# Kernel tuning notes

Hardware: AMD Instinct MI355X
Metric: run time of the kernel (lower is better)

The kernel has to match this reference:

```python
import jax, jax.numpy as jnp
import numpy as np

N_NODES = 100000
D = 128
N_EDGES = 640000


def _spmm(edge_index, w, x, n):
    # out[i] = sum over edges (i<-j): w * x[j]
    src, dst = edge_index[0], edge_index[1]
    return jax.ops.segment_sum(w[:, None] * x[dst], src, num_segments=n)


def setup_inputs() -> dict:
    key = jax.random.key(0)
    ks = jax.random.split(key, 8)
    inp = {
        "index_vectors": jax.random.normal(ks[0], (N_NODES, D), dtype=jnp.float32),
        "edge_index1": jax.random.randint(ks[1], (2, N_EDGES), 0, N_NODES, dtype=jnp.int64),
        "w1": jnp.ones((N_EDGES,), dtype=jnp.float32),
        "edge_index2": jax.random.randint(ks[2], (2, N_EDGES), 0, N_NODES, dtype=jnp.int64),
        "w2": jnp.ones((N_EDGES,), dtype=jnp.float32),
        "edge_index3": jax.random.randint(ks[3], (2, N_EDGES), 0, N_NODES, dtype=jnp.int64),
        "w3": jnp.ones((N_EDGES,), dtype=jnp.float32),
        "zeroth": jax.random.uniform(ks[4], (1, 1), dtype=jnp.float32),
        "fst": jax.random.uniform(ks[5], (1, 1), dtype=jnp.float32),
        "snd": jax.random.uniform(ks[6], (1, 1), dtype=jnp.float32),
        "trd": jax.random.uniform(ks[7], (1, 1), dtype=jnp.float32),
    }
    return inp


def reference(index_vectors, edge_index1, w1, edge_index2, w2, edge_index3, w3,
              zeroth, fst, snd, trd):
    n = index_vectors.shape[0]
    # hop-1 context: A @ x
    fst_ctx = _spmm(edge_index1, w1, index_vectors, n)
    # hop-2 context: A^2 @ roll(x, 1, axis=1)   (permute_vecs=True)
    snd_ctx = _spmm(edge_index2, w2, jnp.roll(index_vectors, 1, axis=1), n)
    # hop-3 context: A^3 @ roll(x, 2, axis=1)
    trd_ctx = _spmm(edge_index3, w3, jnp.roll(index_vectors, 2, axis=1), n)

    # relu-normalized scalar order weights (get_orders)
    r0, r1, r2, r3 = (jax.nn.relu(zeroth), jax.nn.relu(fst),
                      jax.nn.relu(snd), jax.nn.relu(trd))
    tot = r0 + r1 + r2 + r3 + 1e-6
    r0, r1, r2, r3 = r0 / tot, r1 / tot, r2 / tot, r3 / tot

    # use_sign=False -> plain weighted combination
    return r0 * index_vectors + r1 * fst_ctx + r2 * snd_ctx + r3 * trd_ctx
```

## Files before the change

### kernel.cpp

```cpp
#include <hip/hip_runtime.h>

#define N_NODES 100000
#define D 128
#define N_EDGES 640000
#define TOT_EDGES (3 * N_EDGES)

#define NB   256
#define NPB  391
#define BCAP 9216
#define OVF_CAP 65536
#define EPB  3072
#define BINA_BLOCKS (TOT_EDGES / EPB)
#define EPT  (EPB / 256)

#define WS_OVFCNT 0
#define WS_BCUR   64
#define WS_BBASE  16448
#define WS_BNUM   17472
#define WS_OVF    18496
#define WS_TMP    1067072
#define WS_FREC   19941440
#define WS_OFFS   35301440
#define WS_TOTAL_F 35701444

__device__ __forceinline__ void load_r(const float* z0, const float* z1,
                                       const float* z2, const float* z3,
                                       float& r0, float& r1, float& r2, float& r3) {
    r0 = fmaxf(z0[0], 0.0f);
    r1 = fmaxf(z1[0], 0.0f);
    r2 = fmaxf(z2[0], 0.0f);
    r3 = fmaxf(z3[0], 0.0f);
    float inv = 1.0f / (r0 + r1 + r2 + r3 + 1e-6f);
    r0 *= inv; r1 *= inv; r2 *= inv; r3 *= inv;
}

__global__ void binA_kernel(const int* __restrict__ ei1, const float* __restrict__ w1,
                            const int* __restrict__ ei2, const float* __restrict__ w2,
                            const int* __restrict__ ei3, const float* __restrict__ w3,
                            const float* __restrict__ z0, const float* __restrict__ z1,
                            const float* __restrict__ z2, const float* __restrict__ z3,
                            int* __restrict__ bcur, int* __restrict__ ovf_count,
                            int4* __restrict__ ovf, int2* __restrict__ tmp) {
    __shared__ int hist[NB];
    __shared__ int base[NB];
    int t = threadIdx.x;
    hist[t] = 0;
    __syncthreads();

    int e0 = blockIdx.x * EPB;
    int rank[EPT];
    int bkt[EPT];

    for (int k = 0; k < EPT; ++k) {
        int e = e0 + t + k * 256;
        int set = e / N_EDGES;
        int idx = e - set * N_EDGES;
        const int* ei = (set == 0) ? ei1 : (set == 1) ? ei2 : ei3;
        int src = ei[idx];
        int b = src / NPB;
        bkt[k]  = b;
        rank[k] = atomicAdd(&hist[b], 1);
    }
    __syncthreads();

    {
        int h = hist[t];
        base[t] = h ? atomicAdd(&bcur[t * 16], h) : 0;
    }
    __syncthreads();

    float r0, r1, r2, r3;
    load_r(z0, z1, z2, z3, r0, r1, r2, r3);

    for (int k = 0; k < EPT; ++k) {
        int e = e0 + t + k * 256;
        int set = e / N_EDGES;
        int idx = e - set * N_EDGES;
        const int* ei;  const float* w;
        if      (set == 0) { ei = ei1; w = w1; }
        else if (set == 1) { ei = ei2; w = w2; }
        else               { ei = ei3; w = w3; }
        int src = ei[idx];
        int dst = ei[N_EDGES + idx];
        float rk = (set == 0) ? r1 : (set == 1) ? r2 : r3;
        float scale = rk * w[idx];
        int b = bkt[k];
        int local = src - b * NPB;
        int pos = base[b] + rank[k];
        int rx = dst | (set << 17) | (local << 19);
        if (pos < BCAP) {
            tmp[(size_t)b * BCAP + pos] = make_int2(rx, __float_as_int(scale));
        } else {
            int o = atomicAdd(ovf_count, 1);
            if (o < OVF_CAP) ovf[o] = make_int4(src, dst | (set << 17),
                                                __float_as_int(scale), 0);
        }
    }
}

__global__ void scanB_kernel(const int* __restrict__ bcur,
                             int* __restrict__ bbase, int* __restrict__ bnum,
                             int* __restrict__ offsets) {
    __shared__ int s[NB];
    int t = threadIdx.x;
    int n = bcur[t * 16];
    if (n > BCAP) n = BCAP;
    bnum[t] = n;
    s[t] = n;
    __syncthreads();
    for (int off = 1; off < NB; off <<= 1) {
        int v = (t >= off) ? s[t - off] : 0;
        __syncthreads();
        s[t] += v;
        __syncthreads();
    }
    bbase[t] = s[t] - n;
    if (t == NB - 1) offsets[N_NODES] = s[t];
}

__global__ void binB_kernel(const int2* __restrict__ tmp,
                            const int* __restrict__ bbase, const int* __restrict__ bnum,
                            int2* __restrict__ frecs, int* __restrict__ offsets) {
    __shared__ int d[512];
    __shared__ int s[512];
    __shared__ int cur[NPB];
    int b = blockIdx.x;
    int t = threadIdx.x;
    int n = bnum[b];
    int gbase = bbase[b];

    d[t] = 0; d[t + 256] = 0;
    __syncthreads();
    for (int i = t; i < n; i += 256) {
        int rx = tmp[(size_t)b * BCAP + i].x;
        atomicAdd(&d[(rx >> 19) & 0x1FF], 1);
    }
    __syncthreads();
    s[t] = d[t]; s[t + 256] = d[t + 256];
    __syncthreads();
    for (int off = 1; off < 512; off <<= 1) {
        int v0 = (t       >= off) ? s[t       - off] : 0;
        int v1 = (t + 256 >= off) ? s[t + 256 - off] : 0;
        __syncthreads();
        s[t] += v0; s[t + 256] += v1;
        __syncthreads();
    }
    int node0 = b * NPB;
    for (int l = t; l < NPB; l += 256) {
        int excl = s[l] - d[l];
        cur[l] = excl;
        int node = node0 + l;
        if (node < N_NODES) offsets[node] = gbase + excl;
    }
    __syncthreads();
    for (int i = t; i < n; i += 256) {
        int2 rec = tmp[(size_t)b * BCAP + i];
        int pos = atomicAdd(&cur[(rec.x >> 19) & 0x1FF], 1);
        frecs[gbase + pos] = make_int2(rec.x & 0x7FFFF, rec.y);
    }
}

__global__ void gatherd_kernel(const float* __restrict__ x,
                               const int* __restrict__ offsets,
                               const int2* __restrict__ recs,
                               const float* __restrict__ z0, const float* __restrict__ z1,
                               const float* __restrict__ z2, const float* __restrict__ z3,
                               float* __restrict__ out) {
    int wid  = (blockIdx.x * blockDim.x + threadIdx.x) >> 6;
    int lane = threadIdx.x & 63;
    if (wid >= N_NODES) return;

    float r0, r1, r2, r3;
    load_r(z0, z1, z2, z3, r0, r1, r2, r3);

    float2 xv = ((const float2*)(x + (size_t)wid * D))[lane];

    int beg = offsets[wid];
    int end = offsets[wid + 1];
    int count = end - beg;
    int cnt64 = (count < 64) ? count : 64;

    int2 myrec = make_int2(0, 0);
    if (lane < cnt64) myrec = recs[beg + lane];

    float2 a0 = {0.f, 0.f}, a1 = {0.f, 0.f}, a2 = {0.f, 0.f};

    int j = 0;
    for (; j + 3 < cnt64; j += 4) {
        int rxa = __shfl(myrec.x, j),     rya = __shfl(myrec.y, j);
        int rxb = __shfl(myrec.x, j + 1), ryb = __shfl(myrec.y, j + 1);
        int rxc = __shfl(myrec.x, j + 2), ryc = __shfl(myrec.y, j + 2);
        int rxd = __shfl(myrec.x, j + 3), ryd = __shfl(myrec.y, j + 3);
        float2 va = ((const float2*)(x + (size_t)(rxa & 0x1FFFF) * D))[lane];
        float2 vb = ((const float2*)(x + (size_t)(rxb & 0x1FFFF) * D))[lane];
        float2 vc = ((const float2*)(x + (size_t)(rxc & 0x1FFFF) * D))[lane];
        float2 vd = ((const float2*)(x + (size_t)(rxd & 0x1FFFF) * D))[lane];
        int sha = rxa >> 17, shb = rxb >> 17, shc = rxc >> 17, shd = rxd >> 17;
        float sca = __int_as_float(rya), scb = __int_as_float(ryb);
        float scc = __int_as_float(ryc), scd = __int_as_float(ryd);
        if      (sha == 0) { a0.x += sca * va.x; a0.y += sca * va.y; }
        else if (sha == 1) { a1.x += sca * va.x; a1.y += sca * va.y; }
        else               { a2.x += sca * va.x; a2.y += sca * va.y; }
        if      (shb == 0) { a0.x += scb * vb.x; a0.y += scb * vb.y; }
        else if (shb == 1) { a1.x += scb * vb.x; a1.y += scb * vb.y; }
        else               { a2.x += scb * vb.x; a2.y += scb * vb.y; }
        if      (shc == 0) { a0.x += scc * vc.x; a0.y += scc * vc.y; }
        else if (shc == 1) { a1.x += scc * vc.x; a1.y += scc * vc.y; }
        else               { a2.x += scc * vc.x; a2.y += scc * vc.y; }
        if      (shd == 0) { a0.x += scd * vd.x; a0.y += scd * vd.y; }
        else if (shd == 1) { a1.x += scd * vd.x; a1.y += scd * vd.y; }
        else               { a2.x += scd * vd.x; a2.y += scd * vd.y; }
    }
    for (; j < cnt64; ++j) {
        int rx = __shfl(myrec.x, j), ry = __shfl(myrec.y, j);
        float2 v = ((const float2*)(x + (size_t)(rx & 0x1FFFF) * D))[lane];
        int sh = rx >> 17;
        float sc = __int_as_float(ry);
        if      (sh == 0) { a0.x += sc * v.x; a0.y += sc * v.y; }
        else if (sh == 1) { a1.x += sc * v.x; a1.y += sc * v.y; }
        else               { a2.x += sc * v.x; a2.y += sc * v.y; }
    }
    for (int q = 64; q < count; ++q) {
        int2 rec = recs[beg + q];
        float2 v = ((const float2*)(x + (size_t)(rec.x & 0x1FFFF) * D))[lane];
        int sh = rec.x >> 17;
        float sc = __int_as_float(rec.y);
        if      (sh == 0) { a0.x += sc * v.x; a0.y += sc * v.y; }
        else if (sh == 1) { a1.x += sc * v.x; a1.y += sc * v.y; }
        else               { a2.x += sc * v.x; a2.y += sc * v.y; }
    }

    int prev = (lane + 63) & 63;
    float r1y = __shfl(a1.y, prev);
    float r2x = __shfl(a2.x, prev);
    float r2y = __shfl(a2.y, prev);
    float2 o;
    o.x = r0 * xv.x + a0.x + r1y  + r2x;
    o.y = r0 * xv.y + a0.y + a1.x + r2y;
    ((float2*)(out + (size_t)wid * D))[lane] = o;
}

__global__ void ovf_kernel(const float* __restrict__ x,
                           const int* __restrict__ ovf_count,
                           const int4* __restrict__ ovf,
                           float* __restrict__ out) {
    int total_waves = (gridDim.x * blockDim.x) >> 6;
    int gw   = (blockIdx.x * blockDim.x + threadIdx.x) >> 6;
    int lane = threadIdx.x & 63;
    int n = *ovf_count;
    if (n > OVF_CAP) n = OVF_CAP;
    for (int r = gw; r < n; r += total_waves) {
        int4 rec = ovf[r];
        int src = rec.x;
        int dst = rec.y & 0x1FFFF;
        int sh  = (rec.y >> 17) & 3;
        float sc = __int_as_float(rec.z);
        const float* xr = x + (size_t)dst * D;
        float* orow = out + (size_t)src * D;
        int c0 = 2 * lane, c1 = 2 * lane + 1;
        atomicAdd(&orow[c0], sc * xr[(c0 - sh) & 127]);
        atomicAdd(&orow[c1], sc * xr[(c1 - sh) & 127]);
    }
}

#define SCAN_BLOCKS ((N_NODES + 255) / 256)
#define WS_COUNTS   0
#define WS_OFFSETS  400000
#define WS_CURSORS  800008
#define WS_BSUM     1200008
#define WS_BPRE     1201576
#define WS_RECS     1203144
#define WS_NEEDED_MID (WS_RECS + (size_t)TOT_EDGES * 8)

__global__ void hist_kernel(const int* __restrict__ ei1, const int* __restrict__ ei2,
                            const int* __restrict__ ei3, int* __restrict__ counts) {
    int e = blockIdx.x * blockDim.x + threadIdx.x;
    if (e >= TOT_EDGES) return;
    int set = e / N_EDGES;
    int idx = e - set * N_EDGES;
    const int* ei = (set == 0) ? ei1 : (set == 1) ? ei2 : ei3;
    atomicAdd(&counts[ei[idx]], 1);
}

__global__ void scan1_kernel(const int* __restrict__ counts,
                             int* __restrict__ offsets, int* __restrict__ bsum) {
    __shared__ int s[256];
    int t = threadIdx.x;
    int i = blockIdx.x * 256 + t;
    int v = (i < N_NODES) ? counts[i] : 0;
    s[t] = v;
    __syncthreads();
    for (int off = 1; off < 256; off <<= 1) {
        int u = (t >= off) ? s[t - off] : 0;
        __syncthreads();
        s[t] += u;
        __syncthreads();
    }
    if (i < N_NODES) offsets[i] = s[t] - v;
    if (t == 255) bsum[blockIdx.x] = s[255];
}

__global__ void scan2_kernel(const int* __restrict__ bsum, int* __restrict__ bpre) {
    __shared__ int s[512];
    int t = threadIdx.x;
    int v = (t < SCAN_BLOCKS) ? bsum[t] : 0;
    s[t] = v;
    __syncthreads();
    for (int off = 1; off < 512; off <<= 1) {
        int u = (t >= off) ? s[t - off] : 0;
        __syncthreads();
        s[t] += u;
        __syncthreads();
    }
    if (t < SCAN_BLOCKS) bpre[t] = s[t] - v;
}

__global__ void scan3_kernel(int* __restrict__ offsets, const int* __restrict__ bpre,
                             int* __restrict__ cursors) {
    int i = blockIdx.x * 256 + threadIdx.x;
    if (i < N_NODES) {
        int v = offsets[i] + bpre[blockIdx.x];
        offsets[i] = v;
        cursors[i] = v;
    }
    if (i == 0) offsets[N_NODES] = TOT_EDGES;
}

__global__ void fill_kernel(const int* __restrict__ ei1, const float* __restrict__ w1,
                            const int* __restrict__ ei2, const float* __restrict__ w2,
                            const int* __restrict__ ei3, const float* __restrict__ w3,
                            const float* __restrict__ z0, const float* __restrict__ z1,
                            const float* __restrict__ z2, const float* __restrict__ z3,
                            int* __restrict__ cursors, int2* __restrict__ recs) {
    int e = blockIdx.x * blockDim.x + threadIdx.x;
    if (e >= TOT_EDGES) return;
    int set = e / N_EDGES;
    int idx = e - set * N_EDGES;
    const int* ei;  const float* w;
    if      (set == 0) { ei = ei1; w = w1; }
    else if (set == 1) { ei = ei2; w = w2; }
    else               { ei = ei3; w = w3; }
    float r0, r1, r2, r3;
    load_r(z0, z1, z2, z3, r0, r1, r2, r3);
    float rk = (set == 0) ? r1 : (set == 1) ? r2 : r3;
    int src = ei[idx];
    int dst = ei[N_EDGES + idx];
    float scale = rk * w[idx];
    int pos = atomicAdd(&cursors[src], 1);
    recs[pos] = make_int2(dst | (set << 17), __float_as_int(scale));
}

extern "C" void kernel_launch(void* const* d_in, const int* in_sizes, int n_in,
                              void* d_out, int out_size, void* d_ws, size_t ws_size,
                              hipStream_t stream) {
    const float* x   = (const float*)d_in[0];
    const int*   ei1 = (const int*)  d_in[1];
    const float* w1  = (const float*)d_in[2];
    const int*   ei2 = (const int*)  d_in[3];
    const float* w2  = (const float*)d_in[4];
    const int*   ei3 = (const int*)  d_in[5];
    const float* w3  = (const float*)d_in[6];
    const float* z0  = (const float*)d_in[7];
    const float* z1  = (const float*)d_in[8];
    const float* z2  = (const float*)d_in[9];
    const float* z3  = (const float*)d_in[10];
    float* out = (float*)d_out;
    char* wsc = (char*)d_ws;

    if (ws_size >= WS_TOTAL_F) {
        int*  ovf_count = (int*) (wsc + WS_OVFCNT);
        int*  bcur      = (int*) (wsc + WS_BCUR);
        int*  bbase     = (int*) (wsc + WS_BBASE);
        int*  bnum      = (int*) (wsc + WS_BNUM);
        int4* ovf       = (int4*)(wsc + WS_OVF);
        int2* tmp       = (int2*)(wsc + WS_TMP);
        int2* frecs     = (int2*)(wsc + WS_FREC);
        int*  offsets   = (int*) (wsc + WS_OFFS);

        hipMemsetAsync(wsc, 0, WS_BBASE, stream);
        binA_kernel<<<BINA_BLOCKS, 256, 0, stream>>>(ei1, w1, ei2, w2, ei3, w3,
                                                     z0, z1, z2, z3,
                                                     bcur, ovf_count, ovf, tmp);
        scanB_kernel<<<1, NB, 0, stream>>>(bcur, bbase, bnum, offsets);
        binB_kernel<<<NB, 256, 0, stream>>>(tmp, bbase, bnum, frecs, offsets);
        gatherd_kernel<<<(N_NODES * 64 + 255) / 256, 256, 0, stream>>>(x, offsets, frecs,
                                                                       z0, z1, z2, z3, out);
        ovf_kernel<<<128, 256, 0, stream>>>(x, ovf_count, ovf, out);
    } else {
        int*  counts  = (int*) (wsc + WS_COUNTS);
        int*  offsets = (int*) (wsc + WS_OFFSETS);
        int*  cursors = (int*) (wsc + WS_CURSORS);
        int*  bsum    = (int*) (wsc + WS_BSUM);
        int*  bpre    = (int*) (wsc + WS_BPRE);
        int2* recs    = (int2*)(wsc + WS_RECS);

        hipMemsetAsync(counts, 0, N_NODES * sizeof(int), stream);
        hist_kernel<<<TOT_EDGES / 256, 256, 0, stream>>>(ei1, ei2, ei3, counts);
        scan1_kernel<<<SCAN_BLOCKS, 256, 0, stream>>>(counts, offsets, bsum);
        scan2_kernel<<<1, 512, 0, stream>>>(bsum, bpre);
        scan3_kernel<<<SCAN_BLOCKS, 256, 0, stream>>>(offsets, bpre, cursors);
        fill_kernel<<<TOT_EDGES / 256, 256, 0, stream>>>(ei1, w1, ei2, w2, ei3, w3,
                                                         z0, z1, z2, z3, cursors, recs);
        gatherd_kernel<<<(N_NODES * 64 + 255) / 256, 256, 0, stream>>>(x, offsets, recs,
                                                                       z0, z1, z2, z3, out);
    }
}
```

Before: 320.6 us.

## Fuse bucket sort with per-node gather and gather from bf16 copy of x

Merges the second binning pass and the per-node gather into one 1024-thread-per-bucket kernel, so the offsets array and a separate gather launch are no longer needed. A new cast kernel first writes a bf16 copy of x, and neighbour rows are gathered from it at half the bytes. The trade-offs are an extra cast pass over x, only 256 large blocks doing the latency-bound gather, shallower load batching per wave, and lower precision in the gathered context. The workspace requirement also grows, and the fast path only runs if the workspace is large enough.

```diff
diff --git a/kernel.cpp b/kernel.cpp
--- a/kernel.cpp
+++ b/kernel.cpp
@@ -20,8 +20,8 @@
 #define WS_OVF    18496
 #define WS_TMP    1067072
 #define WS_FREC   19941440
-#define WS_OFFS   35301440
-#define WS_TOTAL_F 35701444
+#define WS_XB     35301440
+#define WS_TOTAL_FAST 60901440
 
 __device__ __forceinline__ void load_r(const float* z0, const float* z1,
                                        const float* z2, const float* z3,
@@ -32,6 +32,21 @@
     r3 = fmaxf(z3[0], 0.0f);
     float inv = 1.0f / (r0 + r1 + r2 + r3 + 1e-6f);
     r0 *= inv; r1 *= inv; r2 *= inv; r3 *= inv;
+}
+
+__device__ __forceinline__ unsigned short bf16rn(float f) {
+    unsigned int u = __float_as_uint(f);
+    u += 0x7FFFu + ((u >> 16) & 1u);
+    return (unsigned short)(u >> 16);
+}
+
+__global__ void cast_kernel(const float* __restrict__ x, ushort* __restrict__ xb) {
+    int i = blockIdx.x * 256 + threadIdx.x;
+    if (i >= N_NODES * D / 4) return;
+    float4 v = ((const float4*)x)[i];
+    ushort4 h;
+    h.x = bf16rn(v.x); h.y = bf16rn(v.y); h.z = bf16rn(v.z); h.w = bf16rn(v.w);
+    ((ushort4*)xb)[i] = h;
 }
 
 __global__ void binA_kernel(const int* __restrict__ ei1, const float* __restrict__ w1,
@@ -99,8 +114,7 @@
 }
 
 __global__ void scanB_kernel(const int* __restrict__ bcur,
-                             int* __restrict__ bbase, int* __restrict__ bnum,
-                             int* __restrict__ offsets) {
+                             int* __restrict__ bbase, int* __restrict__ bnum) {
     __shared__ int s[NB];
     int t = threadIdx.x;
     int n = bcur[t * 16];
@@ -115,129 +129,104 @@
         __syncthreads();
     }
     bbase[t] = s[t] - n;
-    if (t == NB - 1) offsets[N_NODES] = s[t];
-}
-
-__global__ void binB_kernel(const int2* __restrict__ tmp,
-                            const int* __restrict__ bbase, const int* __restrict__ bnum,
-                            int2* __restrict__ frecs, int* __restrict__ offsets) {
+}
+
+__global__ __launch_bounds__(1024) void bucket_kernel(
+        const float* __restrict__ x, const ushort* __restrict__ xb,
+        const int2* __restrict__ tmp,
+        const int* __restrict__ bbase, const int* __restrict__ bnum,
+        int2* __restrict__ frecs,
+        const float* __restrict__ z0, const float* __restrict__ z1,
+        const float* __restrict__ z2, const float* __restrict__ z3,
+        float* __restrict__ out) {
     __shared__ int d[512];
     __shared__ int s[512];
-    __shared__ int cur[NPB];
+    __shared__ int cur[512];
     int b = blockIdx.x;
     int t = threadIdx.x;
     int n = bnum[b];
     int gbase = bbase[b];
-
-    d[t] = 0; d[t + 256] = 0;
-    __syncthreads();
-    for (int i = t; i < n; i += 256) {
-        int rx = tmp[(size_t)b * BCAP + i].x;
-        atomicAdd(&d[(rx >> 19) & 0x1FF], 1);
-    }
-    __syncthreads();
-    s[t] = d[t]; s[t + 256] = d[t + 256];
+    const int2* bucket = tmp + (size_t)b * BCAP;
+
+    if (t < 512) d[t] = 0;
+    __syncthreads();
+    for (int i = t; i < n; i += 1024)
+        atomicAdd(&d[(bucket[i].x >> 19) & 0x1FF], 1);
+    __syncthreads();
+    if (t < 512) s[t] = d[t];
     __syncthreads();
     for (int off = 1; off < 512; off <<= 1) {
-        int v0 = (t       >= off) ? s[t       - off] : 0;
-        int v1 = (t + 256 >= off) ? s[t + 256 - off] : 0;
-        __syncthreads();
-        s[t] += v0; s[t + 256] += v1;
-        __syncthreads();
-    }
-    int node0 = b * NPB;
-    for (int l = t; l < NPB; l += 256) {
-        int excl = s[l] - d[l];
-        cur[l] = excl;
-        int node = node0 + l;
-        if (node < N_NODES) offsets[node] = gbase + excl;
-    }
-    __syncthreads();
-    for (int i = t; i < n; i += 256) {
-        int2 rec = tmp[(size_t)b * BCAP + i];
+        int v = 0;
+        if (t < 512 && t >= off) v = s[t - off];
+        __syncthreads();
+        if (t < 512) s[t] += v;
+        __syncthreads();
+    }
+    if (t < 512) cur[t] = s[t] - d[t];
+    __syncthreads();
+    for (int i = t; i < n; i += 1024) {
+        int2 rec = bucket[i];
         int pos = atomicAdd(&cur[(rec.x >> 19) & 0x1FF], 1);
-        frecs[gbase + pos] = make_int2(rec.x & 0x7FFFF, rec.y);
-    }
-}
-
-__global__ void gatherd_kernel(const float* __restrict__ x,
-                               const int* __restrict__ offsets,
-                               const int2* __restrict__ recs,
-                               const float* __restrict__ z0, const float* __restrict__ z1,
-                               const float* __restrict__ z2, const float* __restrict__ z3,
-                               float* __restrict__ out) {
-    int wid  = (blockIdx.x * blockDim.x + threadIdx.x) >> 6;
-    int lane = threadIdx.x & 63;
-    if (wid >= N_NODES) return;
+        frecs[gbase + pos] = rec;
+    }
+    __syncthreads();
 
     float r0, r1, r2, r3;
     load_r(z0, z1, z2, z3, r0, r1, r2, r3);
 
-    float2 xv = ((const float2*)(x + (size_t)wid * D))[lane];
-
-    int beg = offsets[wid];
-    int end = offsets[wid + 1];
-    int count = end - beg;
-    int cnt64 = (count < 64) ? count : 64;
-
-    int2 myrec = make_int2(0, 0);
-    if (lane < cnt64) myrec = recs[beg + lane];
-
-    float2 a0 = {0.f, 0.f}, a1 = {0.f, 0.f}, a2 = {0.f, 0.f};
-
-    int j = 0;
-    for (; j + 3 < cnt64; j += 4) {
-        int rxa = __shfl(myrec.x, j),     rya = __shfl(myrec.y, j);
-        int rxb = __shfl(myrec.x, j + 1), ryb = __shfl(myrec.y, j + 1);
-        int rxc = __shfl(myrec.x, j + 2), ryc = __shfl(myrec.y, j + 2);
-        int rxd = __shfl(myrec.x, j + 3), ryd = __shfl(myrec.y, j + 3);
-        float2 va = ((const float2*)(x + (size_t)(rxa & 0x1FFFF) * D))[lane];
-        float2 vb = ((const float2*)(x + (size_t)(rxb & 0x1FFFF) * D))[lane];
-        float2 vc = ((const float2*)(x + (size_t)(rxc & 0x1FFFF) * D))[lane];
-        float2 vd = ((const float2*)(x + (size_t)(rxd & 0x1FFFF) * D))[lane];
-        int sha = rxa >> 17, shb = rxb >> 17, shc = rxc >> 17, shd = rxd >> 17;
-        float sca = __int_as_float(rya), scb = __int_as_float(ryb);
-        float scc = __int_as_float(ryc), scd = __int_as_float(ryd);
-        if      (sha == 0) { a0.x += sca * va.x; a0.y += sca * va.y; }
-        else if (sha == 1) { a1.x += sca * va.x; a1.y += sca * va.y; }
-        else               { a2.x += sca * va.x; a2.y += sca * va.y; }
-        if      (shb == 0) { a0.x += scb * vb.x; a0.y += scb * vb.y; }
-        else if (shb == 1) { a1.x += scb * vb.x; a1.y += scb * vb.y; }
-        else               { a2.x += scb * vb.x; a2.y += scb * vb.y; }
-        if      (shc == 0) { a0.x += scc * vc.x; a0.y += scc * vc.y; }
-        else if (shc == 1) { a1.x += scc * vc.x; a1.y += scc * vc.y; }
-        else               { a2.x += scc * vc.x; a2.y += scc * vc.y; }
-        if      (shd == 0) { a0.x += scd * vd.x; a0.y += scd * vd.y; }
-        else if (shd == 1) { a1.x += scd * vd.x; a1.y += scd * vd.y; }
-        else               { a2.x += scd * vd.x; a2.y += scd * vd.y; }
-    }
-    for (; j < cnt64; ++j) {
-        int rx = __shfl(myrec.x, j), ry = __shfl(myrec.y, j);
-        float2 v = ((const float2*)(x + (size_t)(rx & 0x1FFFF) * D))[lane];
-        int sh = rx >> 17;
-        float sc = __int_as_float(ry);
-        if      (sh == 0) { a0.x += sc * v.x; a0.y += sc * v.y; }
-        else if (sh == 1) { a1.x += sc * v.x; a1.y += sc * v.y; }
-        else               { a2.x += sc * v.x; a2.y += sc * v.y; }
-    }
-    for (int q = 64; q < count; ++q) {
-        int2 rec = recs[beg + q];
-        float2 v = ((const float2*)(x + (size_t)(rec.x & 0x1FFFF) * D))[lane];
-        int sh = rec.x >> 17;
-        float sc = __int_as_float(rec.y);
-        if      (sh == 0) { a0.x += sc * v.x; a0.y += sc * v.y; }
-        else if (sh == 1) { a1.x += sc * v.x; a1.y += sc * v.y; }
-        else               { a2.x += sc * v.x; a2.y += sc * v.y; }
-    }
-
+    int wave = t >> 6;
+    int lane = t & 63;
     int prev = (lane + 63) & 63;
-    float r1y = __shfl(a1.y, prev);
-    float r2x = __shfl(a2.x, prev);
-    float r2y = __shfl(a2.y, prev);
-    float2 o;
-    o.x = r0 * xv.x + a0.x + r1y  + r2x;
-    o.y = r0 * xv.y + a0.y + a1.x + r2y;
-    ((float2*)(out + (size_t)wid * D))[lane] = o;
+
+    for (int l = wave; l < NPB; l += 16) {
+        int node = b * NPB + l;
+        if (node >= N_NODES) break;
+        int endp = cur[l];
+        int beg  = endp - d[l];
+
+        float2 xv = ((const float2*)(x + (size_t)node * D))[lane];
+        float2 a0 = {0.f, 0.f}, a1 = {0.f, 0.f}, a2 = {0.f, 0.f};
+
+        int j = beg;
+        for (; j + 1 < endp; j += 2) {
+            int2 ra = frecs[gbase + j];
+            int2 rb = frecs[gbase + j + 1];
+            unsigned int va = ((const unsigned int*)(xb + (size_t)(ra.x & 0x1FFFF) * D))[lane];
+            unsigned int vb = ((const unsigned int*)(xb + (size_t)(rb.x & 0x1FFFF) * D))[lane];
+            int sha = (ra.x >> 17) & 3, shb = (rb.x >> 17) & 3;
+            float sca = __int_as_float(ra.y);
+            float scb = __int_as_float(rb.y);
+            float ax = __uint_as_float(va << 16);
+            float ay = __uint_as_float(va & 0xFFFF0000u);
+            float bx = __uint_as_float(vb << 16);
+            float by = __uint_as_float(vb & 0xFFFF0000u);
+            if      (sha == 0) { a0.x += sca * ax; a0.y += sca * ay; }
+            else if (sha == 1) { a1.x += sca * ax; a1.y += sca * ay; }
+            else               { a2.x += sca * ax; a2.y += sca * ay; }
+            if      (shb == 0) { a0.x += scb * bx; a0.y += scb * by; }
+            else if (shb == 1) { a1.x += scb * bx; a1.y += scb * by; }
+            else               { a2.x += scb * bx; a2.y += scb * by; }
+        }
+        if (j < endp) {
+            int2 rec = frecs[gbase + j];
+            unsigned int vv = ((const unsigned int*)(xb + (size_t)(rec.x & 0x1FFFF) * D))[lane];
+            int sh = (rec.x >> 17) & 3;
+            float sc = __int_as_float(rec.y);
+            float vx = __uint_as_float(vv << 16);
+            float vy = __uint_as_float(vv & 0xFFFF0000u);
+            if      (sh == 0) { a0.x += sc * vx; a0.y += sc * vy; }
+            else if (sh == 1) { a1.x += sc * vx; a1.y += sc * vy; }
+            else               { a2.x += sc * vx; a2.y += sc * vy; }
+        }
+
+        float r1y = __shfl(a1.y, prev);
+        float r2x = __shfl(a2.x, prev);
+        float r2y = __shfl(a2.y, prev);
+        float2 o;
+        o.x = r0 * xv.x + a0.x + r1y  + r2x;
+        o.y = r0 * xv.y + a0.y + a1.x + r2y;
+        ((float2*)(out + (size_t)node * D))[lane] = o;
+    }
 }
 
 __global__ void ovf_kernel(const float* __restrict__ x,
@@ -350,6 +339,40 @@
     recs[pos] = make_int2(dst | (set << 17), __float_as_int(scale));
 }
 
+__global__ void gatherd_kernel(const float* __restrict__ x,
+                               const int* __restrict__ offsets,
+                               const int2* __restrict__ recs,
+                               const float* __restrict__ z0, const float* __restrict__ z1,
+                               const float* __restrict__ z2, const float* __restrict__ z3,
+                               float* __restrict__ out) {
+    int wid  = (blockIdx.x * blockDim.x + threadIdx.x) >> 6;
+    int lane = threadIdx.x & 63;
+    if (wid >= N_NODES) return;
+    float r0, r1, r2, r3;
+    load_r(z0, z1, z2, z3, r0, r1, r2, r3);
+    float2 xv = ((const float2*)(x + (size_t)wid * D))[lane];
+    int beg = offsets[wid];
+    int end = offsets[wid + 1];
+    float2 a0 = {0.f, 0.f}, a1 = {0.f, 0.f}, a2 = {0.f, 0.f};
+    for (int j = beg; j < end; ++j) {
+        int2 rec = recs[j];
+        float2 v = ((const float2*)(x + (size_t)(rec.x & 0x1FFFF) * D))[lane];
+        int sh = (rec.x >> 17) & 3;
+        float sc = __int_as_float(rec.y);
+        if      (sh == 0) { a0.x += sc * v.x; a0.y += sc * v.y; }
+        else if (sh == 1) { a1.x += sc * v.x; a1.y += sc * v.y; }
+        else               { a2.x += sc * v.x; a2.y += sc * v.y; }
+    }
+    int prev = (lane + 63) & 63;
+    float r1y = __shfl(a1.y, prev);
+    float r2x = __shfl(a2.x, prev);
+    float r2y = __shfl(a2.y, prev);
+    float2 o;
+    o.x = r0 * xv.x + a0.x + r1y  + r2x;
+    o.y = r0 * xv.y + a0.y + a1.x + r2y;
+    ((float2*)(out + (size_t)wid * D))[lane] = o;
+}
+
 extern "C" void kernel_launch(void* const* d_in, const int* in_sizes, int n_in,
                               void* d_out, int out_size, void* d_ws, size_t ws_size,
                               hipStream_t stream) {
@@ -367,24 +390,24 @@
     float* out = (float*)d_out;
     char* wsc = (char*)d_ws;
 
-    if (ws_size >= WS_TOTAL_F) {
-        int*  ovf_count = (int*) (wsc + WS_OVFCNT);
-        int*  bcur      = (int*) (wsc + WS_BCUR);
-        int*  bbase     = (int*) (wsc + WS_BBASE);
-        int*  bnum      = (int*) (wsc + WS_BNUM);
-        int4* ovf       = (int4*)(wsc + WS_OVF);
-        int2* tmp       = (int2*)(wsc + WS_TMP);
-        int2* frecs     = (int2*)(wsc + WS_FREC);
-        int*  offsets   = (int*) (wsc + WS_OFFS);
+    if (ws_size >= WS_TOTAL_FAST) {
+        int*    ovf_count = (int*)   (wsc + WS_OVFCNT);
+        int*    bcur      = (int*)   (wsc + WS_BCUR);
+        int*    bbase     = (int*)   (wsc + WS_BBASE);
+        int*    bnum      = (int*)   (wsc + WS_BNUM);
+        int4*   ovf       = (int4*)  (wsc + WS_OVF);
+        int2*   tmp       = (int2*)  (wsc + WS_TMP);
+        int2*   frecs     = (int2*)  (wsc + WS_FREC);
+        ushort* xb        = (ushort*)(wsc + WS_XB);
 
         hipMemsetAsync(wsc, 0, WS_BBASE, stream);
+        cast_kernel<<<(N_NODES * D / 4 + 255) / 256, 256, 0, stream>>>(x, xb);
         binA_kernel<<<BINA_BLOCKS, 256, 0, stream>>>(ei1, w1, ei2, w2, ei3, w3,
                                                      z0, z1, z2, z3,
                                                      bcur, ovf_count, ovf, tmp);
-        scanB_kernel<<<1, NB, 0, stream>>>(bcur, bbase, bnum, offsets);
-        binB_kernel<<<NB, 256, 0, stream>>>(tmp, bbase, bnum, frecs, offsets);
-        gatherd_kernel<<<(N_NODES * 64 + 255) / 256, 256, 0, stream>>>(x, offsets, frecs,
-                                                                       z0, z1, z2, z3, out);
+        scanB_kernel<<<1, NB, 0, stream>>>(bcur, bbase, bnum);
+        bucket_kernel<<<NB, 1024, 0, stream>>>(x, xb, tmp, bbase, bnum, frecs,
+                                               z0, z1, z2, z3, out);
         ovf_kernel<<<128, 256, 0, stream>>>(x, ovf_count, ovf, out);
     } else {
         int*  counts  = (int*) (wsc + WS_COUNTS);
```

Measured after the change: 386.8 us. 20.6% more time.
